# Kernel optimization log

Measured on AMD Instinct MI355X. Metric: run time of the kernel, lower is better.

The kernel has to match this reference:

```python
import jax, jax.numpy as jnp
import numpy as np

N_EMBD = 1024
N_HEAD = 16
HEAD = N_EMBD // N_HEAD
D_FF = 4 * N_EMBD
B, T = 2, 2048


def setup_inputs() -> dict:
    key = jax.random.key(0)
    ks = jax.random.split(key, 12)
    s = 0.02
    return {
        "x": jax.random.normal(ks[0], (B, T, N_EMBD), jnp.float32),
        "Wq": jax.random.normal(ks[1], (N_EMBD, N_EMBD), jnp.float32) * s,
        "bq": jnp.zeros((N_EMBD,), jnp.float32),
        "Wk": jax.random.normal(ks[2], (N_EMBD, N_EMBD), jnp.float32) * s,
        "bk": jnp.zeros((N_EMBD,), jnp.float32),
        "Wv": jax.random.normal(ks[3], (N_EMBD, N_EMBD), jnp.float32) * s,
        "bv": jnp.zeros((N_EMBD,), jnp.float32),
        "Wo": jax.random.normal(ks[4], (N_EMBD, N_EMBD), jnp.float32) * s,
        "bo": jnp.zeros((N_EMBD,), jnp.float32),
        "W1": jax.random.normal(ks[5], (N_EMBD, D_FF), jnp.float32) * s,
        "b1": jnp.zeros((D_FF,), jnp.float32),
        "W2": jax.random.normal(ks[6], (D_FF, N_EMBD), jnp.float32) * s,
        "b2": jnp.zeros((N_EMBD,), jnp.float32),
        "g1": jnp.ones((N_EMBD,), jnp.float32),
        "be1": jnp.zeros((N_EMBD,), jnp.float32),
        "g2": jnp.ones((N_EMBD,), jnp.float32),
        "be2": jnp.zeros((N_EMBD,), jnp.float32),
    }


def _layernorm(x, g, b, eps=1e-3):
    # keras LayerNormalization default epsilon=1e-3
    mu = jnp.mean(x, axis=-1, keepdims=True)
    var = jnp.mean(jnp.square(x - mu), axis=-1, keepdims=True)
    return (x - mu) * jax.lax.rsqrt(var + eps) * g + b


def _attention(h, Wq, bq, Wk, bk, Wv, bv, Wo, bo):
    b, t, _ = h.shape
    q = (h @ Wq + bq).reshape(b, t, N_HEAD, HEAD)
    k = (h @ Wk + bk).reshape(b, t, N_HEAD, HEAD)
    v = (h @ Wv + bv).reshape(b, t, N_HEAD, HEAD)
    scores = jnp.einsum("bthd,bshd->bhts", q, k) / jnp.sqrt(jnp.float32(HEAD))
    causal = jnp.tril(jnp.ones((t, t), bool))
    scores = jnp.where(causal, scores, -jnp.inf)
    w = jax.nn.softmax(scores, axis=-1)  # dropout is identity in eval
    ctx = jnp.einsum("bhts,bshd->bthd", w, v).reshape(b, t, N_EMBD)
    return ctx @ Wo + bo


def reference(x, Wq, bq, Wk, bk, Wv, bv, Wo, bo, W1, b1, W2, b2, g1, be1, g2, be2):
    x = x + _attention(_layernorm(x, g1, be1), Wq, bq, Wk, bk, Wv, bv, Wo, bo)
    h = _layernorm(x, g2, be2)
    ff = jax.nn.relu(h @ W1 + b1) @ W2 + b2
    return x + ff
```

## Files before the change

### kernel.cpp

```cpp
#include <hip/hip_runtime.h>

typedef __bf16 bf16;
typedef __attribute__((ext_vector_type(8))) __bf16 bf16x8;
typedef __attribute__((ext_vector_type(4))) __bf16 bf16x4;
typedef __attribute__((ext_vector_type(4))) float f32x4;

#define MFMA16(A, B, C) __builtin_amdgcn_mfma_f32_16x16x32_bf16(A, B, C, 0, 0, 0)

#define GLOAD16(gp, lp)                                          \
  __builtin_amdgcn_global_load_lds(                              \
      (const __attribute__((address_space(1))) void*)(gp),       \
      (__attribute__((address_space(3))) void*)(lp), 16, 0, 0)

__device__ __forceinline__ float fexp2(float x) {
#if __has_builtin(__builtin_amdgcn_exp2f)
  return __builtin_amdgcn_exp2f(x);
#else
  float r;
  asm("v_exp_f32 %0, %1" : "=v"(r) : "v"(x));
  return r;
#endif
}

#define QSCL 0.18033688011112042f

__global__ __launch_bounds__(256) void transpose_cvt_kernel(
    const float* __restrict__ in, bf16* __restrict__ out, int K, int N)
{
  __shared__ float tile[32][33];
  const int kt = blockIdx.y * 32;
  const int nt = blockIdx.x * 32;
  const int tx = threadIdx.x, ty = threadIdx.y;
#pragma unroll
  for (int j = 0; j < 4; ++j)
    tile[ty + j * 8][tx] = in[(size_t)(kt + ty + j * 8) * N + nt + tx];
  __syncthreads();
#pragma unroll
  for (int j = 0; j < 4; ++j)
    out[(size_t)(nt + ty + j * 8) * K + kt + tx] = (bf16)tile[tx][ty + j * 8];
}

__global__ __launch_bounds__(256) void transpose4_cvt_kernel(
    const float* __restrict__ w0, const float* __restrict__ w1,
    const float* __restrict__ w2, const float* __restrict__ w3,
    bf16* __restrict__ out)
{
  __shared__ float tile[32][33];
  const float* srcs[4] = {w0, w1, w2, w3};
  const float* in = srcs[blockIdx.z];
  bf16* o = out + (size_t)blockIdx.z * 1024 * 1024;
  const int kt = blockIdx.y * 32;
  const int nt = blockIdx.x * 32;
  const int tx = threadIdx.x, ty = threadIdx.y;
#pragma unroll
  for (int j = 0; j < 4; ++j)
    tile[ty + j * 8][tx] = in[(size_t)(kt + ty + j * 8) * 1024 + nt + tx];
  __syncthreads();
#pragma unroll
  for (int j = 0; j < 4; ++j)
    o[(size_t)(nt + ty + j * 8) * 1024 + kt + tx] = (bf16)tile[tx][ty + j * 8];
}

__global__ __launch_bounds__(256) void ln_kernel(
    const float* __restrict__ in, const float* __restrict__ gamma,
    const float* __restrict__ beta, bf16* __restrict__ out)
{
  const int row = blockIdx.x;
  const int t = threadIdx.x;
  const float4 v = ((const float4*)(in + (size_t)row * 1024))[t];
  float s = v.x + v.y + v.z + v.w;
  float sq = v.x * v.x + v.y * v.y + v.z * v.z + v.w * v.w;
#pragma unroll
  for (int m = 1; m < 64; m <<= 1) {
    s += __shfl_xor(s, m);
    sq += __shfl_xor(sq, m);
  }
  __shared__ float ssum[4], ssq[4];
  const int w = t >> 6;
  if ((t & 63) == 0) { ssum[w] = s; ssq[w] = sq; }
  __syncthreads();
  s = ssum[0] + ssum[1] + ssum[2] + ssum[3];
  sq = ssq[0] + ssq[1] + ssq[2] + ssq[3];
  const float mu = s * (1.0f / 1024.0f);
  const float var = sq * (1.0f / 1024.0f) - mu * mu;
  const float rs = rsqrtf(var + 1e-3f);
  const float4 g = ((const float4*)gamma)[t];
  const float4 b = ((const float4*)beta)[t];
  bf16x4 o;
  o[0] = (bf16)((v.x - mu) * rs * g.x + b.x);
  o[1] = (bf16)((v.y - mu) * rs * g.y + b.y);
  o[2] = (bf16)((v.z - mu) * rs * g.z + b.z);
  o[3] = (bf16)((v.w - mu) * rs * g.w + b.w);
  *(bf16x4*)(out + (size_t)row * 1024 + t * 4) = o;
}

template <int BM, int BN, int BK, int EPI, int SWZ>
__global__ __launch_bounds__(256, 2) void gemm_bt(
    const bf16* __restrict__ A, const bf16* __restrict__ Bt,
    const float* __restrict__ bias0, const float* __restrict__ bias1,
    const float* __restrict__ bias2, const float* __restrict__ resid,
    bf16* __restrict__ out0, bf16* __restrict__ out1, bf16* __restrict__ out2,
    float* __restrict__ outf, int M, int N, int K)
{
  constexpr int WM = BM / 2, WN = BN / 2;
  constexpr int MI = WM / 16, NJ = WN / 16;
  constexpr int KK = BK / 32;
  constexpr int NSLOT = BK / 8;
  constexpr int SMASK = NSLOT - 1;
  constexpr int RPL = 512 / BK;
  constexpr int ALOADS = BM / (4 * RPL);
  constexpr int BLOADS = BN / (4 * RPL);
  constexpr int S = ALOADS + BLOADS;

  __shared__ bf16 As[3][BM * BK];
  __shared__ bf16 Bs[3][BN * BK];
  const int tid = threadIdx.x;
  const int lane = tid & 63, w = tid >> 6;
  const int wr = w >> 1, wc = w & 1;
  const int g = lane >> 4, lr = lane & 15;

  int bx = blockIdx.x, by = blockIdx.y;
  if constexpr (SWZ) {
    const int bid = bx + gridDim.x * by;
    const int xcd = bid & 7, idx = bid >> 3;
    const int chunk = gridDim.y >> 3;
    by = xcd * chunk + (idx % chunk);
    bx = idx / chunk;
  }
  const int brow = by * BM, bcol = bx * BN;

  f32x4 acc[MI][NJ] = {};

  const int lrow = lane / NSLOT;
  const int slot = lane & SMASK;
  int lcol;
  if constexpr (BK == 32)
    lcol = ((slot - (lrow >> 1)) & 3) * 8;
  else
    lcol = (slot ^ (lrow & 7)) * 8;

  auto stage = [&](int buf, int k0) {
#pragma unroll
    for (int j = 0; j < ALOADS; ++j) {
      const int row0 = w * (BM / 4) + j * RPL;
      GLOAD16(A + (size_t)(brow + row0 + lrow) * K + k0 + lcol,
              &As[buf][row0 * BK]);
    }
#pragma unroll
    for (int j = 0; j < BLOADS; ++j) {
      const int row0 = w * (BN / 4) + j * RPL;
      GLOAD16(Bt + (size_t)(bcol + row0 + lrow) * K + k0 + lcol,
              &Bs[buf][row0 * BK]);
    }
  };

  auto rdslot = [&](int kg) {
    if constexpr (BK == 32) return ((kg + (lr >> 1)) & 3) * 8;
    else return (kg ^ (lr & 7)) * 8;
  };

  const int nk = K / BK;
  stage(0, 0);
  stage(1, BK);
  int cur = 0;
  for (int t = 0; t < nk; ++t) {
    if (t + 1 < nk) {
      if constexpr (S == 3)
        asm volatile("s_waitcnt vmcnt(3)" ::: "memory");
      else if constexpr (S == 4)
        asm volatile("s_waitcnt vmcnt(4)" ::: "memory");
      else
        asm volatile("s_waitcnt vmcnt(6)" ::: "memory");
    } else {
      asm volatile("s_waitcnt vmcnt(0)" ::: "memory");
    }
    __builtin_amdgcn_s_barrier();
    __builtin_amdgcn_sched_barrier(0);

    bf16x8 afr[MI][KK], bfr[NJ][KK];
#pragma unroll
    for (int i = 0; i < MI; ++i)
#pragma unroll
      for (int kk = 0; kk < KK; ++kk)
        afr[i][kk] = *(const bf16x8*)&As[cur][(wr * WM + i * 16 + lr) * BK +
                                             rdslot(kk * 4 + g)];
#pragma unroll
    for (int j = 0; j < NJ; ++j)
#pragma unroll
      for (int kk = 0; kk < KK; ++kk)
        bfr[j][kk] = *(const bf16x8*)&Bs[cur][(wc * WN + j * 16 + lr) * BK +
                                             rdslot(kk * 4 + g)];

    if (t + 2 < nk) {
      int nb = cur + 2;
      if (nb >= 3) nb -= 3;
      stage(nb, (t + 2) * BK);
    }

    __builtin_amdgcn_s_setprio(1);
#pragma unroll
    for (int kk = 0; kk < KK; ++kk)
#pragma unroll
      for (int i = 0; i < MI; ++i)
#pragma unroll
        for (int j = 0; j < NJ; ++j)
          acc[i][j] = MFMA16(afr[i][kk], bfr[j][kk], acc[i][j]);
    __builtin_amdgcn_s_setprio(0);

    ++cur;
    if (cur == 3) cur = 0;
  }

#pragma unroll
  for (int i = 0; i < MI; ++i) {
#pragma unroll
    for (int j = 0; j < NJ; ++j) {
      const int r0 = brow + wr * WM + i * 16 + g * 4;
      const int c = bcol + wc * WN + j * 16 + lr;
      if constexpr (EPI == 1) {
        const float bv = bias0[c];
#pragma unroll
        for (int rr = 0; rr < 4; ++rr)
          out0[(size_t)(r0 + rr) * N + c] =
              (bf16)fmaxf(acc[i][j][rr] + bv, 0.0f);
      } else if constexpr (EPI == 2) {
        const float bv = bias0[c];
#pragma unroll
        for (int rr = 0; rr < 4; ++rr) {
          const size_t idx = (size_t)(r0 + rr) * N + c;
          outf[idx] = acc[i][j][rr] + bv + resid[idx];
        }
      } else {
        const int sub = c >> 10;
        const int c1 = c & 1023;
        if (sub == 0) {
          const float bv = bias0[c1];
#pragma unroll
          for (int rr = 0; rr < 4; ++rr)
            out0[(size_t)(r0 + rr) * 1024 + c1] =
                (bf16)((acc[i][j][rr] + bv) * QSCL);
        } else if (sub == 1) {
          const float bv = bias1[c1];
#pragma unroll
          for (int rr = 0; rr < 4; ++rr)
            out1[(size_t)(r0 + rr) * 1024 + c1] = (bf16)(acc[i][j][rr] + bv);
        } else {
          const float bv = bias2[c1];
          const int bb = r0 >> 11, t0 = r0 & 2047;
          const int hh = c1 >> 6, dd = c1 & 63;
          bf16x4 pk;
#pragma unroll
          for (int rr = 0; rr < 4; ++rr) pk[rr] = (bf16)(acc[i][j][rr] + bv);
          *(bf16x4*)(out2 + ((size_t)((bb * 16 + hh) * 64 + dd)) * 2048 + t0) = pk;
        }
      }
    }
  }
}

__global__ __launch_bounds__(256) void attn_kernel(
    const bf16* __restrict__ q, const bf16* __restrict__ kmat,
    const bf16* __restrict__ vt, bf16* __restrict__ ctx)
{
  __shared__ bf16 Ks[64 * 64];
  __shared__ bf16 Vs[64 * 64];
  __shared__ bf16 Pq[4][16][88];
  const int bx = blockIdx.x, by = blockIdx.y;
  const int qt = (by & 16) ? (31 - ((bx + by - 16) & 31)) : ((bx + by) & 31);
  const int b_ = by >> 4, h_ = by & 15;
  const int qb = qt * 64;
  const int tid = threadIdx.x;
  const int lane = tid & 63, w = tid >> 6;
  const int g = lane >> 4, lr = lane & 15;
  const int qrow = qb + w * 16 + lr;

  bf16x8 qf[2];
  {
    const bf16* qp = q + (size_t)(b_ * 2048 + qrow) * 1024 + h_ * 64 + g * 8;
    qf[0] = *(const bf16x8*)qp;
    qf[1] = *(const bf16x8*)(qp + 32);
  }

  f32x4 o[4] = {};
  float l = 0.f;

  const int srow = tid >> 2;
  const int c16 = (tid & 3) * 16;
  const int rb = srow * 128;
  const int sw = (srow & 7) << 4;
  const bf16* kbase = kmat + (size_t)(b_ * 2048) * 1024 + h_ * 64;
  const bf16* vbase = vt + (size_t)(b_ * 16 + h_) * 64 * 2048;
  const bf16* kp0 = kbase + (size_t)srow * 1024 + c16;
  const bf16* vp0 = vbase + (size_t)srow * 2048 + c16;

  bf16x8 k0 = *(const bf16x8*)kp0;
  bf16x8 k1 = *(const bf16x8*)(kp0 + 8);
  bf16x8 v0 = *(const bf16x8*)vp0;
  bf16x8 v1 = *(const bf16x8*)(vp0 + 8);

  for (int s0 = 0; s0 <= qb; s0 += 64) {
    *(bf16x8*)((char*)Ks + ((rb + c16 * 2) ^ sw)) = k0;
    *(bf16x8*)((char*)Ks + ((rb + c16 * 2 + 16) ^ sw)) = k1;
    *(bf16x8*)((char*)Vs + ((rb + c16 * 2) ^ sw)) = v0;
    *(bf16x8*)((char*)Vs + ((rb + c16 * 2 + 16) ^ sw)) = v1;
    __syncthreads();
    if (s0 < qb) {
      const bf16* kp = kp0 + (size_t)(s0 + 64) * 1024;
      k0 = *(const bf16x8*)kp;
      k1 = *(const bf16x8*)(kp + 8);
      const bf16* vp = vp0 + (s0 + 64);
      v0 = *(const bf16x8*)vp;
      v1 = *(const bf16x8*)(vp + 8);
    }

    f32x4 st[4];
    __builtin_amdgcn_s_setprio(1);
#pragma unroll
    for (int n = 0; n < 4; ++n) {
      f32x4 z = {};
#pragma unroll
      for (int kk = 0; kk < 2; ++kk) {
        const int row = n * 16 + lr;
        bf16x8 ak = *(const bf16x8*)((char*)Ks +
            ((row * 128 + kk * 64 + g * 16) ^ ((lr & 7) << 4)));
        z = MFMA16(ak, qf[kk], z);
      }
      st[n] = z;
    }
    __builtin_amdgcn_s_setprio(0);

    if (s0 == qb) {
#pragma unroll
      for (int n = 0; n < 4; ++n)
#pragma unroll
        for (int r = 0; r < 4; ++r)
          if (s0 + n * 16 + g * 4 + r > qrow) st[n][r] = -1e30f;
    }

    float rs = 0.f;
#pragma unroll
    for (int n = 0; n < 4; ++n) {
      bf16x4 pk;
#pragma unroll
      for (int r = 0; r < 4; ++r) {
        const float p = fexp2(st[n][r]);
        rs += p;
        pk[r] = (bf16)p;
      }
      *(bf16x4*)&Pq[w][lr][n * 16 + g * 4] = pk;
    }

    bf16x8 pa[2];
#pragma unroll
    for (int kk = 0; kk < 2; ++kk)
      pa[kk] = *(const bf16x8*)&Pq[w][lr][kk * 32 + g * 8];
    __builtin_amdgcn_s_setprio(1);
#pragma unroll
    for (int n = 0; n < 4; ++n) {
      const int row = n * 16 + lr;
#pragma unroll
      for (int kk = 0; kk < 2; ++kk) {
        bf16x8 bv = *(const bf16x8*)((char*)Vs +
            ((row * 128 + kk * 64 + g * 16) ^ ((lr & 7) << 4)));
        o[n] = MFMA16(pa[kk], bv, o[n]);
      }
    }
    __builtin_amdgcn_s_setprio(0);

    rs += __shfl_xor(rs, 16);
    rs += __shfl_xor(rs, 32);
    l += rs;
    __syncthreads();
  }

  float lq[4];
#pragma unroll
  for (int r = 0; r < 4; ++r) lq[r] = __shfl(l, g * 4 + r);
#pragma unroll
  for (int r = 0; r < 4; ++r) {
    const float inv = 1.0f / lq[r];
#pragma unroll
    for (int n = 0; n < 4; ++n)
      ctx[(size_t)(b_ * 2048 + qb + w * 16 + g * 4 + r) * 1024 + h_ * 64 + n * 16 + lr] =
          (bf16)(o[n][r] * inv);
  }
}

extern "C" void kernel_launch(void* const* d_in, const int* in_sizes, int n_in,
                              void* d_out, int out_size, void* d_ws, size_t ws_size,
                              hipStream_t stream)
{
  (void)in_sizes; (void)n_in; (void)out_size; (void)ws_size;
  const float* x   = (const float*)d_in[0];
  const float* Wq  = (const float*)d_in[1];
  const float* bq  = (const float*)d_in[2];
  const float* Wk  = (const float*)d_in[3];
  const float* bk  = (const float*)d_in[4];
  const float* Wv  = (const float*)d_in[5];
  const float* bv  = (const float*)d_in[6];
  const float* Wo  = (const float*)d_in[7];
  const float* bo  = (const float*)d_in[8];
  const float* W1  = (const float*)d_in[9];
  const float* b1  = (const float*)d_in[10];
  const float* W2  = (const float*)d_in[11];
  const float* b2  = (const float*)d_in[12];
  const float* g1  = (const float*)d_in[13];
  const float* be1 = (const float*)d_in[14];
  const float* g2  = (const float*)d_in[15];
  const float* be2 = (const float*)d_in[16];
  float* out = (float*)d_out;

  char* ws = (char*)d_ws;
  const size_t MB = 1024 * 1024;
  bf16* wqkv_t = (bf16*)(ws + 0 * MB);
  bf16* wo_t = (bf16*)(ws + 6 * MB);
  bf16* w1_t = (bf16*)(ws + 8 * MB);
  bf16* w2_t = (bf16*)(ws + 16 * MB);
  bf16* h1   = (bf16*)(ws + 24 * MB);
  bf16* qbuf = (bf16*)(ws + 32 * MB);
  bf16* kbuf = (bf16*)(ws + 40 * MB);
  bf16* vtb  = (bf16*)(ws + 48 * MB);
  bf16* ctx  = (bf16*)(ws + 56 * MB);
  bf16* h2   = (bf16*)(ws + 64 * MB);
  bf16* ff1  = (bf16*)(ws + 24 * MB);

  const dim3 tb(32, 8);
  transpose4_cvt_kernel<<<dim3(32, 32, 4), tb, 0, stream>>>(
      Wq, Wk, Wv, Wo, wqkv_t);
  transpose_cvt_kernel<<<dim3(128, 32), tb, 0, stream>>>(W1, w1_t, 1024, 4096);
  transpose_cvt_kernel<<<dim3(32, 128), tb, 0, stream>>>(W2, w2_t, 4096, 1024);

  ln_kernel<<<4096, 256, 0, stream>>>(x, g1, be1, h1);

  gemm_bt<128, 128, 32, 4, 0><<<dim3(24, 32), 256, 0, stream>>>(
      h1, wqkv_t, bq, bk, bv, nullptr, qbuf, kbuf, vtb, nullptr, 4096, 3072, 1024);

  attn_kernel<<<dim3(32, 32), 256, 0, stream>>>(qbuf, kbuf, vtb, ctx);

  gemm_bt<128, 64, 64, 2, 0><<<dim3(16, 32), 256, 0, stream>>>(
      ctx, wo_t, bo, nullptr, nullptr, x, nullptr, nullptr, nullptr, out,
      4096, 1024, 1024);

  ln_kernel<<<4096, 256, 0, stream>>>(out, g2, be2, h2);

  gemm_bt<256, 128, 32, 1, 0><<<dim3(32, 16), 256, 0, stream>>>(
      h2, w1_t, b1, nullptr, nullptr, nullptr, ff1, nullptr, nullptr, nullptr,
      4096, 4096, 1024);

  gemm_bt<128, 64, 64, 2, 1><<<dim3(16, 32), 256, 0, stream>>>(
      ff1, w2_t, b2, nullptr, nullptr, out, nullptr, nullptr, nullptr, out,
      4096, 1024, 4096);
}
```

Baseline: 200.7 us.

## Store attention residual in bf16 and remap attention causal tile order

The out-projection GEMM now writes the post-attention residual stream as bf16 instead of fp32. A new bf16-input layernorm reads that buffer, and the final FFN GEMM reads the bf16 residual back and writes fp32 output. This halves the residual traffic between stages but drops the intermediate residual precision to bf16. The attention kernel also uses a new mapping from block to query tile, meant to balance causal work across CUs.

```diff
diff --git a/kernel.cpp b/kernel.cpp
--- a/kernel.cpp
+++ b/kernel.cpp
@@ -94,11 +94,46 @@
   *(bf16x4*)(out + (size_t)row * 1024 + t * 4) = o;
 }
 
+__global__ __launch_bounds__(256) void ln_b_kernel(
+    const bf16* __restrict__ in, const float* __restrict__ gamma,
+    const float* __restrict__ beta, bf16* __restrict__ out)
+{
+  const int row = blockIdx.x;
+  const int t = threadIdx.x;
+  const bf16x4 vb = *(const bf16x4*)(in + (size_t)row * 1024 + t * 4);
+  float v0 = (float)vb[0], v1 = (float)vb[1], v2 = (float)vb[2], v3 = (float)vb[3];
+  float s = v0 + v1 + v2 + v3;
+  float sq = v0 * v0 + v1 * v1 + v2 * v2 + v3 * v3;
+#pragma unroll
+  for (int m = 1; m < 64; m <<= 1) {
+    s += __shfl_xor(s, m);
+    sq += __shfl_xor(sq, m);
+  }
+  __shared__ float ssum[4], ssq[4];
+  const int w = t >> 6;
+  if ((t & 63) == 0) { ssum[w] = s; ssq[w] = sq; }
+  __syncthreads();
+  s = ssum[0] + ssum[1] + ssum[2] + ssum[3];
+  sq = ssq[0] + ssq[1] + ssq[2] + ssq[3];
+  const float mu = s * (1.0f / 1024.0f);
+  const float var = sq * (1.0f / 1024.0f) - mu * mu;
+  const float rs = rsqrtf(var + 1e-3f);
+  const float4 g = ((const float4*)gamma)[t];
+  const float4 b = ((const float4*)beta)[t];
+  bf16x4 o;
+  o[0] = (bf16)((v0 - mu) * rs * g.x + b.x);
+  o[1] = (bf16)((v1 - mu) * rs * g.y + b.y);
+  o[2] = (bf16)((v2 - mu) * rs * g.z + b.z);
+  o[3] = (bf16)((v3 - mu) * rs * g.w + b.w);
+  *(bf16x4*)(out + (size_t)row * 1024 + t * 4) = o;
+}
+
 template <int BM, int BN, int BK, int EPI, int SWZ>
 __global__ __launch_bounds__(256, 2) void gemm_bt(
     const bf16* __restrict__ A, const bf16* __restrict__ Bt,
     const float* __restrict__ bias0, const float* __restrict__ bias1,
     const float* __restrict__ bias2, const float* __restrict__ resid,
+    const bf16* __restrict__ residb,
     bf16* __restrict__ out0, bf16* __restrict__ out1, bf16* __restrict__ out2,
     float* __restrict__ outf, int M, int N, int K)
 {
@@ -223,12 +258,19 @@
         for (int rr = 0; rr < 4; ++rr)
           out0[(size_t)(r0 + rr) * N + c] =
               (bf16)fmaxf(acc[i][j][rr] + bv, 0.0f);
-      } else if constexpr (EPI == 2) {
+      } else if constexpr (EPI == 5) {
         const float bv = bias0[c];
 #pragma unroll
         for (int rr = 0; rr < 4; ++rr) {
           const size_t idx = (size_t)(r0 + rr) * N + c;
-          outf[idx] = acc[i][j][rr] + bv + resid[idx];
+          out0[idx] = (bf16)(acc[i][j][rr] + bv + resid[idx]);
+        }
+      } else if constexpr (EPI == 6) {
+        const float bv = bias0[c];
+#pragma unroll
+        for (int rr = 0; rr < 4; ++rr) {
+          const size_t idx = (size_t)(r0 + rr) * N + c;
+          outf[idx] = acc[i][j][rr] + bv + (float)residb[idx];
         }
       } else {
         const int sub = c >> 10;
@@ -266,7 +308,11 @@
   __shared__ bf16 Vs[64 * 64];
   __shared__ bf16 Pq[4][16][88];
   const int bx = blockIdx.x, by = blockIdx.y;
-  const int qt = (by & 16) ? (31 - ((bx + by - 16) & 31)) : ((bx + by) & 31);
+  const int k4 = by >> 3;
+  const int qt = (k4 == 0) ? bx
+               : (k4 == 1) ? (31 - bx)
+               : (k4 == 2) ? (bx ^ 16)
+                           : (31 - (bx ^ 16));
   const int b_ = by >> 4, h_ = by & 15;
   const int qb = qt * 64;
   const int tid = threadIdx.x;
@@ -422,6 +468,7 @@
   bf16* vtb  = (bf16*)(ws + 48 * MB);
   bf16* ctx  = (bf16*)(ws + 56 * MB);
   bf16* h2   = (bf16*)(ws + 64 * MB);
+  bf16* x2b  = (bf16*)(ws + 72 * MB);
   bf16* ff1  = (bf16*)(ws + 24 * MB);
 
   const dim3 tb(32, 8);
@@ -433,21 +480,22 @@
   ln_kernel<<<4096, 256, 0, stream>>>(x, g1, be1, h1);
 
   gemm_bt<128, 128, 32, 4, 0><<<dim3(24, 32), 256, 0, stream>>>(
-      h1, wqkv_t, bq, bk, bv, nullptr, qbuf, kbuf, vtb, nullptr, 4096, 3072, 1024);
+      h1, wqkv_t, bq, bk, bv, nullptr, nullptr, qbuf, kbuf, vtb, nullptr,
+      4096, 3072, 1024);
 
   attn_kernel<<<dim3(32, 32), 256, 0, stream>>>(qbuf, kbuf, vtb, ctx);
 
-  gemm_bt<128, 64, 64, 2, 0><<<dim3(16, 32), 256, 0, stream>>>(
-      ctx, wo_t, bo, nullptr, nullptr, x, nullptr, nullptr, nullptr, out,
-      4096, 1024, 1024);
-
-  ln_kernel<<<4096, 256, 0, stream>>>(out, g2, be2, h2);
+  gemm_bt<128, 64, 64, 5, 0><<<dim3(16, 32), 256, 0, stream>>>(
+      ctx, wo_t, bo, nullptr, nullptr, x, nullptr, x2b, nullptr, nullptr,
+      nullptr, 4096, 1024, 1024);
+
+  ln_b_kernel<<<4096, 256, 0, stream>>>(x2b, g2, be2, h2);
 
   gemm_bt<256, 128, 32, 1, 0><<<dim3(32, 16), 256, 0, stream>>>(
-      h2, w1_t, b1, nullptr, nullptr, nullptr, ff1, nullptr, nullptr, nullptr,
-      4096, 4096, 1024);
-
-  gemm_bt<128, 64, 64, 2, 1><<<dim3(16, 32), 256, 0, stream>>>(
-      ff1, w2_t, b2, nullptr, nullptr, out, nullptr, nullptr, nullptr, out,
-      4096, 1024, 4096);
-}
+      h2, w1_t, b1, nullptr, nullptr, nullptr, nullptr, ff1, nullptr, nullptr,
+      nullptr, 4096, 4096, 1024);
+
+  gemm_bt<128, 64, 64, 6, 1><<<dim3(16, 32), 256, 0, stream>>>(
+      ff1, w2_t, b2, nullptr, nullptr, nullptr, x2b, nullptr, nullptr, nullptr,
+      out, 4096, 1024, 4096);
+}
```

Measured after the change: 199.8 us. Within noise of the previous version (-0.4%).
